# Optimization experiments

Hardware: AMD Instinct MI355X
Metric: run time of the kernel (lower is better)

The kernel has to match this reference:

```python
import jax, jax.numpy as jnp
import numpy as np

NUM_HEADS = 16
LN_EPS = 1e-5


def setup_inputs() -> dict:
    key = jax.random.key(0)
    ks = jax.random.split(key, 7)
    B, S, D = 4, 1024, 1024
    s_in = 1.0 / np.sqrt(D)
    return {
        "x": jax.random.normal(ks[0], (B, S, D), dtype=jnp.float32),
        # PyTorch MHA packed in-projection: [3D, D] weight, [3D] bias
        "w_qkv": jax.random.uniform(ks[1], (3 * D, D), dtype=jnp.float32, minval=-s_in, maxval=s_in),
        "b_qkv": jnp.zeros((3 * D,), dtype=jnp.float32),
        "w_out": jax.random.uniform(ks[2], (D, D), dtype=jnp.float32, minval=-s_in, maxval=s_in),
        "b_out": jnp.zeros((D,), dtype=jnp.float32),
        "ln_w": jnp.ones((D,), dtype=jnp.float32),
        "ln_b": jnp.zeros((D,), dtype=jnp.float32),
    }


def _layernorm(x, w, b):
    m = jnp.mean(x, axis=-1, keepdims=True)
    v = jnp.var(x, axis=-1, keepdims=True)
    return (x - m) * jax.lax.rsqrt(v + LN_EPS) * w + b


def reference(x, w_qkv, b_qkv, w_out, b_out, ln_w, ln_b):
    B, S, D = x.shape
    H = NUM_HEADS
    hd = D // H
    # packed QKV projection (torch: F.linear(x, w_qkv, b_qkv) then chunk)
    qkv = x @ w_qkv.T + b_qkv                      # [B, S, 3D]
    q, k, v = jnp.split(qkv, 3, axis=-1)
    q = q.reshape(B, S, H, hd).transpose(0, 2, 1, 3) * (hd ** -0.5)  # [B,H,S,hd]
    k = k.reshape(B, S, H, hd).transpose(0, 2, 1, 3)
    v = v.reshape(B, S, H, hd).transpose(0, 2, 1, 3)
    scores = jnp.einsum('bhqd,bhkd->bhqk', q, k)   # [B,H,S,S]
    attn = jax.nn.softmax(scores, axis=-1)
    ctx = jnp.einsum('bhqk,bhkd->bhqd', attn, v)   # [B,H,S,hd]
    ctx = ctx.transpose(0, 2, 1, 3).reshape(B, S, D)
    attn_out = ctx @ w_out.T + b_out
    # torch returns head-averaged weights (average_attn_weights=True)
    attn_weights = attn.mean(axis=1)               # [B,S,S]
    # dropout rate 0.0 -> identity; residual + LayerNorm
    y = _layernorm(x + attn_out, ln_w, ln_b)
    return y, attn_weights
```

## Files before the change

kernel.cpp:

```cpp
#include <hip/hip_runtime.h>
#include <cstdint>

typedef __bf16 bf16;
typedef __bf16 bf16x8 __attribute__((ext_vector_type(8)));
typedef __bf16 bf16x4 __attribute__((ext_vector_type(4)));
typedef float  f32x4  __attribute__((ext_vector_type(4)));

#define MFMA_BF16(a, b, c) __builtin_amdgcn_mfma_f32_16x16x32_bf16(a, b, c, 0, 0, 0)

#define WAITCNT_VM(n) asm volatile("s_waitcnt vmcnt(" #n ")" ::: "memory")
#define CFENCE()      asm volatile("" ::: "memory")

__device__ __forceinline__ void async_load16(const void* g, void* l) {
    __builtin_amdgcn_global_load_lds(
        (__attribute__((address_space(1))) uint32_t*)(uintptr_t)g,
        (__attribute__((address_space(3))) uint32_t*)(uint32_t)(uintptr_t)l,
        16, 0, 0);
}

__global__ void cvt_kernel(const float* __restrict__ src, bf16* __restrict__ dst, int n4) {
    int i = blockIdx.x * blockDim.x + threadIdx.x;
    if (i < n4) {
        float4 v = ((const float4*)src)[i];
        bf16x4 o;
        o[0] = (bf16)v.x; o[1] = (bf16)v.y; o[2] = (bf16)v.z; o[3] = (bf16)v.w;
        ((bf16x4*)dst)[i] = o;
    }
}

__global__ __launch_bounds__(256) void gemm_qkv_kernel(
    const bf16* __restrict__ A, const bf16* __restrict__ W,
    const float* __restrict__ bias,
    bf16* __restrict__ Qb, bf16* __restrict__ Kb, bf16* __restrict__ Vt)
{
    const int Kd = 1024;
    __shared__ bf16 sA[2][128 * 32];
    __shared__ bf16 sB[2][128 * 32];
    int tid = threadIdx.x, lane = tid & 63, wid = tid >> 6;
    int m0 = blockIdx.y * 128, n0 = blockIdx.x * 128;
    int srow = wid * 32 + (lane >> 2);
    int pchunk = lane & 3;
    int jchunk = pchunk ^ ((lane >> 3) & 3);
    const bf16* Ag = A + (size_t)(m0 + srow) * Kd + jchunk * 8;
    const bf16* Wg = W + (size_t)(n0 + srow) * Kd + jchunk * 8;
    int soff = srow * 32 + pchunk * 8;
    int wm = (wid & 1) * 64, wn = (wid >> 1) * 64;
    int lcol = lane & 15, quad = lane >> 4;
    int ckey = (lcol >> 1) & 3;
    f32x4 acc[4][4] = {};
#define STG_Q(buf, k0_) do { \
        async_load16(Ag + (k0_), &sA[buf][soff]); \
        async_load16(Ag + (k0_) + 16 * Kd, &sA[buf][soff + 512]); \
        async_load16(Wg + (k0_), &sB[buf][soff]); \
        async_load16(Wg + (k0_) + 16 * Kd, &sB[buf][soff + 512]); \
    } while (0)
    STG_Q(0, 0);
    STG_Q(1, 32);
    for (int it = 0; it < 32; ++it) {
        if (it < 31) { WAITCNT_VM(4); } else { WAITCNT_VM(0); }
        __builtin_amdgcn_s_barrier();
        CFENCE();
        const bf16* cA = sA[it & 1];
        const bf16* cB = sB[it & 1];
        bf16x8 af[4], bfr[4];
#pragma unroll
        for (int i = 0; i < 4; i++)
            af[i] = *(const bf16x8*)&cA[(wm + i * 16 + lcol) * 32 + (quad ^ ckey) * 8];
#pragma unroll
        for (int i = 0; i < 4; i++)
            bfr[i] = *(const bf16x8*)&cB[(wn + i * 16 + lcol) * 32 + (quad ^ ckey) * 8];
#pragma unroll
        for (int i = 0; i < 4; i++)
#pragma unroll
            for (int j = 0; j < 4; j++)
                acc[i][j] = MFMA_BF16(af[i], bfr[j], acc[i][j]);
        CFENCE();
        __builtin_amdgcn_s_barrier();
        if (it + 2 < 32) STG_Q(it & 1, (it + 2) * 32);
    }
#undef STG_Q
#pragma unroll
    for (int j = 0; j < 4; j++) {
        int n = n0 + wn + j * 16 + lcol;
        float bv = bias[n];
        int part = n >> 10, d = n & 1023, h = d >> 6, dd = d & 63;
#pragma unroll
        for (int i = 0; i < 4; i++) {
            int mb = m0 + wm + i * 16 + quad * 4;
            int b = mb >> 10, s = mb & 1023;
            if (part == 2) {
                bf16x4 v4;
#pragma unroll
                for (int r = 0; r < 4; r++) v4[r] = (bf16)(acc[i][j][r] + bv);
                *(bf16x4*)&Vt[(size_t)((b * 16 + h) * 64 + dd) * 1024 + s] = v4;
            } else {
                float scv = (part == 0) ? 0.125f : 1.0f;
                bf16* dst = (part == 0 ? Qb : Kb) + (size_t)((b * 16 + h) * 1024 + s) * 64 + dd;
#pragma unroll
                for (int r = 0; r < 4; r++) dst[(size_t)r * 64] = (bf16)((acc[i][j][r] + bv) * scv);
            }
        }
    }
}

__global__ __launch_bounds__(256) void gemm_out_kernel(
    const bf16* __restrict__ A, const bf16* __restrict__ W,
    const float* __restrict__ bias, float* __restrict__ out)
{
    const int Kd = 1024;
    __shared__ bf16 sA[2][64 * 32];
    __shared__ bf16 sB[2][128 * 32];
    int tid = threadIdx.x, lane = tid & 63, wid = tid >> 6;
    int m0 = blockIdx.y * 64, n0 = blockIdx.x * 128;
    int ra = tid >> 2;
    int pchunk = tid & 3;
    int jchunk = pchunk ^ ((tid >> 3) & 3);
    const bf16* Ag = A + (size_t)(m0 + ra) * Kd + jchunk * 8;
    const bf16* Wg = W + (size_t)(n0 + ra) * Kd + jchunk * 8;
    int aoff = ra * 32 + pchunk * 8;
    int wm = (wid & 1) * 32, wn = (wid >> 1) * 64;
    int lcol = lane & 15, quad = lane >> 4;
    int ckey = (lcol >> 1) & 3;
    f32x4 acc[2][4] = {};
#define STG_O(buf, k0_) do { \
        async_load16(Ag + (k0_), &sA[buf][aoff]); \
        async_load16(Wg + (k0_), &sB[buf][aoff]); \
        async_load16(Wg + (k0_) + 64 * Kd, &sB[buf][aoff + 64 * 32]); \
    } while (0)
    STG_O(0, 0);
    STG_O(1, 32);
    for (int it = 0; it < 32; ++it) {
        if (it < 31) { WAITCNT_VM(3); } else { WAITCNT_VM(0); }
        __builtin_amdgcn_s_barrier();
        CFENCE();
        const bf16* cA = sA[it & 1];
        const bf16* cB = sB[it & 1];
        bf16x8 af[2], bfr[4];
#pragma unroll
        for (int i = 0; i < 2; i++)
            af[i] = *(const bf16x8*)&cA[(wm + i * 16 + lcol) * 32 + (quad ^ ckey) * 8];
#pragma unroll
        for (int j = 0; j < 4; j++)
            bfr[j] = *(const bf16x8*)&cB[(wn + j * 16 + lcol) * 32 + (quad ^ ckey) * 8];
#pragma unroll
        for (int i = 0; i < 2; i++)
#pragma unroll
            for (int j = 0; j < 4; j++)
                acc[i][j] = MFMA_BF16(af[i], bfr[j], acc[i][j]);
        CFENCE();
        __builtin_amdgcn_s_barrier();
        if (it + 2 < 32) STG_O(it & 1, (it + 2) * 32);
    }
#undef STG_O
#pragma unroll
    for (int j = 0; j < 4; j++) {
        int n = n0 + wn + j * 16 + lcol;
        float bv = bias[n];
#pragma unroll
        for (int i = 0; i < 2; i++) {
            int m = m0 + wm + i * 16 + quad * 4;
#pragma unroll
            for (int r = 0; r < 4; r++) out[(size_t)(m + r) * 1024 + n] = acc[i][j][r] + bv;
        }
    }
}

__global__ __launch_bounds__(256) void flash_kernel(
    const bf16* __restrict__ Qb, const bf16* __restrict__ Kb, const bf16* __restrict__ Vt,
    bf16* __restrict__ ctx, float* __restrict__ ml)
{
    __shared__ bf16 sK[2][64 * 64];
    __shared__ bf16 sV[2][64 * 64];
    __shared__ bf16 pt[4][16 * 64];
    int tid = threadIdx.x, lane = tid & 63, wid = tid >> 6;
    int bx = blockIdx.x;
    int orig = (bx & 7) * 128 + (bx >> 3);
    int qt = orig & 15;
    int h = (orig >> 4) & 15;
    int b = orig >> 8;
    int lcol = lane & 15, quad = lane >> 4;
    size_t base = (size_t)(b * 16 + h) * 65536;

    int q0 = qt * 64 + wid * 16;
    const bf16* qp = Qb + base + (size_t)(q0 + lcol) * 64 + quad * 8;
    bf16x8 a0 = *(const bf16x8*)qp;
    bf16x8 a1 = *(const bf16x8*)(qp + 32);

    char* wpt = (char*)&pt[wid][0];
    int rr8 = lane >> 3;
    int pp  = lane & 7;
    int jj  = pp ^ rr8;
    int sr0 = wid * 16 + rr8;
    int sw  = lcol & 7;

#define STAGE_KV(buf, kt_) do { \
        async_load16(Kb + base + (size_t)((kt_) * 64 + sr0) * 64 + jj * 8,       &sK[buf][sr0 * 64 + pp * 8]); \
        async_load16(Kb + base + (size_t)((kt_) * 64 + sr0 + 8) * 64 + jj * 8,   &sK[buf][(sr0 + 8) * 64 + pp * 8]); \
        async_load16(Vt + base + (size_t)sr0 * 1024 + (kt_) * 64 + jj * 8,       &sV[buf][sr0 * 64 + pp * 8]); \
        async_load16(Vt + base + (size_t)(sr0 + 8) * 1024 + (kt_) * 64 + jj * 8, &sV[buf][(sr0 + 8) * 64 + pp * 8]); \
    } while (0)

    float l_[4] = {0.f, 0.f, 0.f, 0.f};
    f32x4 o[4] = {};

    STAGE_KV(0, 0);
    int cur = 0;
    for (int kt = 0; kt < 16; kt++) {
        __syncthreads();
        if (kt < 15) STAGE_KV(cur ^ 1, kt + 1);
        const bf16* sKc = &sK[cur][0];
        const bf16* sVc = &sV[cur][0];
#pragma unroll
        for (int nt = 0; nt < 4; nt++) {
            int ck = quad ^ sw;
            bf16x8 bk0 = *(const bf16x8*)&sKc[(nt * 16 + lcol) * 64 + ck * 8];
            bf16x8 bk1 = *(const bf16x8*)&sKc[(nt * 16 + lcol) * 64 + (ck ^ 4) * 8];
            f32x4 s = {};
            s = MFMA_BF16(a0, bk0, s);
            s = MFMA_BF16(a1, bk1, s);
#pragma unroll
            for (int rr = 0; rr < 4; rr++) {
                float p = __expf(s[rr]);
                l_[rr] += p;
                int row = quad * 4 + rr;
                *(bf16*)(wpt + row * 128 + ((nt * 32 + lcol * 2) ^ ((row & 7) << 4))) = (bf16)p;
            }
        }
#pragma unroll
        for (int kf = 0; kf < 2; kf++) {
            bf16x8 pa = *(const bf16x8*)(wpt + lcol * 128 + (((kf * 4 + quad) ^ sw) << 4));
#pragma unroll
            for (int dt = 0; dt < 4; dt++) {
                bf16x8 vb = *(const bf16x8*)&sVc[(dt * 16 + lcol) * 64 + ((kf * 4 + quad) ^ sw) * 8];
                o[dt] = MFMA_BF16(pa, vb, o[dt]);
            }
        }
        cur ^= 1;
    }
#undef STAGE_KV
#pragma unroll
    for (int mk = 1; mk < 16; mk <<= 1)
#pragma unroll
        for (int rr = 0; rr < 4; rr++) l_[rr] += __shfl_xor(l_[rr], mk, 64);
#pragma unroll
    for (int rr = 0; rr < 4; rr++) {
        float inv = 1.f / l_[rr];
        int qg = q0 + quad * 4 + rr;
#pragma unroll
        for (int dt = 0; dt < 4; dt++)
            ctx[(size_t)(b * 1024 + qg) * 1024 + h * 64 + dt * 16 + lcol] = (bf16)(o[dt][rr] * inv);
        if (lcol == 0)
            ml[(size_t)(b * 16 + h) * 1024 + qg] = l_[rr];
    }
}

__global__ __launch_bounds__(256) void aw_kernel(
    const bf16* __restrict__ Qb, const bf16* __restrict__ Kb,
    const float* __restrict__ ml, float* __restrict__ aw)
{
    __shared__ bf16 sK[2][64 * 64];
    int tid = threadIdx.x, lane = tid & 63, wid = tid >> 6;
    int bx = blockIdx.x;
    int orig = (bx & 7) * 128 + (bx >> 3);
    int kt = orig & 15;
    int qt = (orig >> 4) & 15;
    int b = orig >> 8;
    int lcol = lane & 15, quad = lane >> 4;
    int q0 = qt * 64 + wid * 16;
    int kbase = kt * 64;
    int sw = lcol & 7;
    int r0_ = tid >> 3, p0_ = tid & 7, j0_ = p0_ ^ (r0_ & 7);
    int r1_ = (tid + 256) >> 3, p1_ = (tid + 256) & 7, j1_ = p1_ ^ (r1_ & 7);

#define STAGE_K(buf, hh) do { \
        size_t hb_ = (size_t)(b * 16 + (hh)) * 65536; \
        async_load16(Kb + hb_ + (size_t)(kbase + r0_) * 64 + j0_ * 8, &sK[buf][(size_t)tid * 8]); \
        async_load16(Kb + hb_ + (size_t)(kbase + r1_) * 64 + j1_ * 8, &sK[buf][(size_t)(tid + 256) * 8]); \
    } while (0)

    float acc[16];
#pragma unroll
    for (int i = 0; i < 16; i++) acc[i] = 0.f;

    STAGE_K(0, 0);
    int cur = 0;
    for (int h = 0; h < 16; h++) {
        size_t base = (size_t)(b * 16 + h) * 65536;
        const bf16* qp = Qb + base + (size_t)(q0 + lcol) * 64 + quad * 8;
        bf16x8 a0 = *(const bf16x8*)qp;
        bf16x8 a1 = *(const bf16x8*)(qp + 32);
        float scale[4];
#pragma unroll
        for (int rr = 0; rr < 4; rr++)
            scale[rr] = 0.0625f / ml[(size_t)(b * 16 + h) * 1024 + q0 + quad * 4 + rr];
        __syncthreads();
        if (h < 15) STAGE_K(cur ^ 1, h + 1);
#pragma unroll
        for (int nt = 0; nt < 4; nt++) {
            int ck = quad ^ sw;
            bf16x8 bk0 = *(const bf16x8*)&sK[cur][(nt * 16 + lcol) * 64 + ck * 8];
            bf16x8 bk1 = *(const bf16x8*)&sK[cur][(nt * 16 + lcol) * 64 + (ck ^ 4) * 8];
            f32x4 s = {};
            s = MFMA_BF16(a0, bk0, s);
            s = MFMA_BF16(a1, bk1, s);
#pragma unroll
            for (int rr = 0; rr < 4; rr++)
                acc[nt * 4 + rr] += __expf(s[rr]) * scale[rr];
        }
        cur ^= 1;
    }
#undef STAGE_K
#pragma unroll
    for (int nt = 0; nt < 4; nt++)
#pragma unroll
        for (int rr = 0; rr < 4; rr++)
            aw[(size_t)(b * 1024 + q0 + quad * 4 + rr) * 1024 + kbase + nt * 16 + lcol] = acc[nt * 4 + rr];
}

__global__ __launch_bounds__(256) void ln_kernel(
    const float* __restrict__ x, const float* __restrict__ ao,
    const float* __restrict__ w, const float* __restrict__ bsh,
    float* __restrict__ y)
{
    int row = blockIdx.x, tid = threadIdx.x;
    float4 xv = ((const float4*)(x + (size_t)row * 1024))[tid];
    float4 av = ((const float4*)(ao + (size_t)row * 1024))[tid];
    float4 v = {xv.x + av.x, xv.y + av.y, xv.z + av.z, xv.w + av.w};
    float s = v.x + v.y + v.z + v.w;
    float ss = v.x * v.x + v.y * v.y + v.z * v.z + v.w * v.w;
#pragma unroll
    for (int off = 32; off; off >>= 1) { s += __shfl_down(s, off); ss += __shfl_down(ss, off); }
    __shared__ float rs[4], rss[4];
    int lane = tid & 63, wid = tid >> 6;
    if (lane == 0) { rs[wid] = s; rss[wid] = ss; }
    __syncthreads();
    s = rs[0] + rs[1] + rs[2] + rs[3];
    ss = rss[0] + rss[1] + rss[2] + rss[3];
    float mean = s * (1.f / 1024.f);
    float var = ss * (1.f / 1024.f) - mean * mean;
    float inv = rsqrtf(var + 1e-5f);
    float4 wv = ((const float4*)w)[tid];
    float4 bv = ((const float4*)bsh)[tid];
    float4 o;
    o.x = (v.x - mean) * inv * wv.x + bv.x;
    o.y = (v.y - mean) * inv * wv.y + bv.y;
    o.z = (v.z - mean) * inv * wv.z + bv.z;
    o.w = (v.w - mean) * inv * wv.w + bv.w;
    ((float4*)y)[row * 256 + tid] = o;
}

extern "C" void kernel_launch(void* const* d_in, const int* in_sizes, int n_in,
                              void* d_out, int out_size, void* d_ws, size_t ws_size,
                              hipStream_t stream) {
    const float* x     = (const float*)d_in[0];
    const float* w_qkv = (const float*)d_in[1];
    const float* b_qkv = (const float*)d_in[2];
    const float* w_out = (const float*)d_in[3];
    const float* b_out = (const float*)d_in[4];
    const float* ln_w  = (const float*)d_in[5];
    const float* ln_b  = (const float*)d_in[6];

    char* ws = (char*)d_ws;
    bf16*   Qb    = (bf16*)(ws);
    bf16*   Kb    = (bf16*)(ws + (8ull  << 20));
    bf16*   Vt    = (bf16*)(ws + (16ull << 20));
    bf16*   ctx   = (bf16*)(ws + (24ull << 20));
    float*  ml    = (float*)(ws + (32ull << 20));
    bf16*   x_bf  = (bf16*)(ws + (33ull << 20));
    bf16*   wq_bf = (bf16*)(ws + (41ull << 20));
    bf16*   wo_bf = (bf16*)(ws + (16ull << 20));
    float*  ao    = (float*)(ws);

    float* y_out  = (float*)d_out;
    float* aw_out = y_out + 4ull * 1024 * 1024;

    cvt_kernel<<<4096, 256, 0, stream>>>(x, x_bf, 1048576);
    cvt_kernel<<<3072, 256, 0, stream>>>(w_qkv, wq_bf, 786432);
    gemm_qkv_kernel<<<dim3(24, 32), 256, 0, stream>>>(x_bf, wq_bf, b_qkv, Qb, Kb, Vt);
    flash_kernel<<<1024, 256, 0, stream>>>(Qb, Kb, Vt, ctx, ml);
    aw_kernel<<<1024, 256, 0, stream>>>(Qb, Kb, ml, aw_out);
    cvt_kernel<<<1024, 256, 0, stream>>>(w_out, wo_bf, 262144);
    gemm_out_kernel<<<dim3(8, 64), 256, 0, stream>>>(ctx, wo_bf, b_out, ao);
    ln_kernel<<<4096, 256, 0, stream>>>(x, ao, ln_w, ln_b, y_out);
}
```

Baseline: 219.5 us.

## Triple-buffer GEMM LDS staging and remap QKV block order for locality

Both projection GEMMs move from double to triple-buffered async global-to-LDS staging, keeping two K-tiles in flight with adjusted vmcnt waits to hide more memory latency. The QKV GEMM also remaps its block index so consecutive blocks are spread across groups of eight, aiming at better L2 reuse or XCD distribution of the A and W tiles. This costs more LDS per block, which can reduce occupancy, and the remap hard-codes a 32x24 grid.

```diff
diff --git a/kernel.cpp b/kernel.cpp
--- a/kernel.cpp
+++ b/kernel.cpp
@@ -34,10 +34,12 @@
     bf16* __restrict__ Qb, bf16* __restrict__ Kb, bf16* __restrict__ Vt)
 {
     const int Kd = 1024;
-    __shared__ bf16 sA[2][128 * 32];
-    __shared__ bf16 sB[2][128 * 32];
+    __shared__ bf16 sA[3][128 * 32];
+    __shared__ bf16 sB[3][128 * 32];
     int tid = threadIdx.x, lane = tid & 63, wid = tid >> 6;
-    int m0 = blockIdx.y * 128, n0 = blockIdx.x * 128;
+    int flat = blockIdx.y * 24 + blockIdx.x;
+    int orig = (flat & 7) * 96 + (flat >> 3);
+    int m0 = (orig / 24) * 128, n0 = (orig % 24) * 128;
     int srow = wid * 32 + (lane >> 2);
     int pchunk = lane & 3;
     int jchunk = pchunk ^ ((lane >> 3) & 3);
@@ -56,12 +58,16 @@
     } while (0)
     STG_Q(0, 0);
     STG_Q(1, 32);
+    STG_Q(2, 64);
+    int cur = 0;
     for (int it = 0; it < 32; ++it) {
-        if (it < 31) { WAITCNT_VM(4); } else { WAITCNT_VM(0); }
+        if (it < 30)      { WAITCNT_VM(8); }
+        else if (it == 30){ WAITCNT_VM(4); }
+        else              { WAITCNT_VM(0); }
         __builtin_amdgcn_s_barrier();
         CFENCE();
-        const bf16* cA = sA[it & 1];
-        const bf16* cB = sB[it & 1];
+        const bf16* cA = sA[cur];
+        const bf16* cB = sB[cur];
         bf16x8 af[4], bfr[4];
 #pragma unroll
         for (int i = 0; i < 4; i++)
@@ -76,7 +82,8 @@
                 acc[i][j] = MFMA_BF16(af[i], bfr[j], acc[i][j]);
         CFENCE();
         __builtin_amdgcn_s_barrier();
-        if (it + 2 < 32) STG_Q(it & 1, (it + 2) * 32);
+        if (it + 3 < 32) STG_Q(cur, (it + 3) * 32);
+        cur = (cur == 2) ? 0 : cur + 1;
     }
 #undef STG_Q
 #pragma unroll
@@ -108,8 +115,8 @@
     const float* __restrict__ bias, float* __restrict__ out)
 {
     const int Kd = 1024;
-    __shared__ bf16 sA[2][64 * 32];
-    __shared__ bf16 sB[2][128 * 32];
+    __shared__ bf16 sA[3][64 * 32];
+    __shared__ bf16 sB[3][128 * 32];
     int tid = threadIdx.x, lane = tid & 63, wid = tid >> 6;
     int m0 = blockIdx.y * 64, n0 = blockIdx.x * 128;
     int ra = tid >> 2;
@@ -129,12 +136,16 @@
     } while (0)
     STG_O(0, 0);
     STG_O(1, 32);
+    STG_O(2, 64);
+    int cur = 0;
     for (int it = 0; it < 32; ++it) {
-        if (it < 31) { WAITCNT_VM(3); } else { WAITCNT_VM(0); }
+        if (it < 30)      { WAITCNT_VM(6); }
+        else if (it == 30){ WAITCNT_VM(3); }
+        else              { WAITCNT_VM(0); }
         __builtin_amdgcn_s_barrier();
         CFENCE();
-        const bf16* cA = sA[it & 1];
-        const bf16* cB = sB[it & 1];
+        const bf16* cA = sA[cur];
+        const bf16* cB = sB[cur];
         bf16x8 af[2], bfr[4];
 #pragma unroll
         for (int i = 0; i < 2; i++)
@@ -149,7 +160,8 @@
                 acc[i][j] = MFMA_BF16(af[i], bfr[j], acc[i][j]);
         CFENCE();
         __builtin_amdgcn_s_barrier();
-        if (it + 2 < 32) STG_O(it & 1, (it + 2) * 32);
+        if (it + 3 < 32) STG_O(cur, (it + 3) * 32);
+        cur = (cur == 2) ? 0 : cur + 1;
     }
 #undef STG_O
 #pragma unroll
```

New measurement: 218.1 us. No clear change (-0.6%).
